# Optimization experiments

Hardware: AMD Instinct MI355X
Metric: run time of the kernel (lower is better)

Reference implementation:

```python
import jax, jax.numpy as jnp
import numpy as np
import functools

N_QUBITS = 4
N_LAYERS = 2
DIM = 2 ** N_QUBITS  # 16


def _cx_full(c, t, n):
    # Full 2^n x 2^n CX(control=c, target=t); Qiskit ordering: qubit 0 = LSB,
    # so kron list is ordered qubit n-1 (leftmost) ... qubit 0 (rightmost).
    P0 = np.diag([1.0, 0.0]); P1 = np.diag([0.0, 1.0])
    X = np.array([[0.0, 1.0], [1.0, 0.0]])
    ops0 = [np.eye(2)] * n; ops0[n - 1 - c] = P0
    ops1 = [np.eye(2)] * n; ops1[n - 1 - c] = P1; ops1[n - 1 - t] = X
    return functools.reduce(np.kron, ops0) + functools.reduce(np.kron, ops1)

# CX chain: CX(0,1), CX(1,2), CX(2,3) applied in circuit order (last applied is leftmost)
_chain = np.eye(DIM)
for _i in range(N_QUBITS - 1):
    _chain = _cx_full(_i, _i + 1, N_QUBITS) @ _chain
CX_CHAIN = jnp.asarray(_chain, dtype=jnp.complex64)
# Odd-pair CX: i in range(1, n_qubits-1, 2)
_odd = np.eye(DIM)
for _i in range(1, N_QUBITS - 1, 2):
    _odd = _cx_full(_i, _i + 1, N_QUBITS) @ _odd
CX_ODD = jnp.asarray(_odd, dtype=jnp.complex64)


def _ry(t):
    c = jnp.cos(t / 2); s = jnp.sin(t / 2)
    return jnp.stack([jnp.stack([c, -s]), jnp.stack([s, c])]).astype(jnp.complex64)


def _rz(t):
    tc = t.astype(jnp.complex64)
    return jnp.diag(jnp.stack([jnp.exp(-0.5j * tc), jnp.exp(0.5j * tc)]))


def _stage(gate_fn, thetas):
    # thetas[i] acts on qubit i; kron ordered qubit n-1 ... qubit 0 (LSB rightmost)
    mats = [gate_fn(thetas[q]) for q in range(N_QUBITS - 1, -1, -1)]
    return functools.reduce(jnp.kron, mats)


def _layer_unitary(theta):
    # theta: (3*N_QUBITS,); per qubit i: RY(theta[3i]) ... RZ(theta[3i+1]) ... RY(theta[3i+2])
    ry_a = _stage(_ry, theta[0::3])
    rz_b = _stage(_rz, theta[1::3])
    ry_c = _stage(_ry, theta[2::3])
    return ry_c @ CX_ODD @ rz_b @ CX_CHAIN @ ry_a


def _quantum_mp(qf, mp_params):
    # qf: (N, n_qubits) real encoded features -> per-node statevector simulation
    v = qf / (jnp.linalg.norm(qf, axis=1, keepdims=True) + 1e-8)
    state = jnp.pad(v, ((0, 0), (0, DIM - N_QUBITS)))  # (N, 16)
    state = state / (jnp.linalg.norm(state, axis=1, keepdims=True) + 1e-8)
    state = state / jnp.linalg.norm(state, axis=1, keepdims=True)
    state = state.astype(jnp.complex64)
    for layer in range(N_LAYERS):
        U = _layer_unitary(mp_params[layer * 3 * N_QUBITS:(layer + 1) * 3 * N_QUBITS])
        state = state @ U.T  # batched U @ |psi>
    return state[:, :N_QUBITS].real.astype(jnp.float32)


def setup_inputs() -> dict:
    key = jax.random.key(0)
    ks = jax.random.split(key, 11)
    N, D_IN, HID = 10000, 256, 128
    return {
        "node_features": jax.random.normal(ks[0], (N, D_IN), jnp.float32),
        "adjacency": jax.random.randint(ks[1], (N, N), 0, 2, jnp.int32),
        "W_e1": jax.random.normal(ks[2], (D_IN, HID), jnp.float32) * 0.05,
        "b_e1": jax.random.normal(ks[3], (HID,), jnp.float32) * 0.05,
        "W_e2": jax.random.normal(ks[4], (HID, N_QUBITS), jnp.float32) * 0.05,
        "b_e2": jax.random.normal(ks[5], (N_QUBITS,), jnp.float32) * 0.05,
        "mp_params": jax.random.normal(ks[6], (N_LAYERS * 3 * N_QUBITS,), jnp.float32) * 0.1,
        "W_d1": jax.random.normal(ks[7], (N_QUBITS, HID), jnp.float32) * 0.05,
        "b_d1": jax.random.normal(ks[8], (HID,), jnp.float32) * 0.05,
        "W_d2": jax.random.normal(ks[9], (HID, HID), jnp.float32) * 0.05,
        "b_d2": jax.random.normal(ks[10], (HID,), jnp.float32) * 0.05,
    }


def reference(node_features, adjacency, W_e1, b_e1, W_e2, b_e2, mp_params, W_d1, b_d1, W_d2, b_d2):
    # Encoder: Linear -> ReLU -> Linear  => (N, n_qubits)
    qf = jnp.maximum(node_features @ W_e1 + b_e1, 0.0) @ W_e2 + b_e2
    # torch detaches both the encoded features and mp_params before the quantum sim
    qf = jax.lax.stop_gradient(qf)
    theta = jax.lax.stop_gradient(mp_params)
    # NOTE: aggregate_neighbors ignores neighbor_states entirely, so adjacency
    # does not influence the output (faithful to the source module).
    updated = _quantum_mp(qf, theta)  # (N, n_qubits)
    h = jnp.maximum(updated @ W_d1 + b_d1, 0.0)
    return h @ W_d2 + b_d2
```

## Files before the change

kernel.cpp:

```cpp
#include <hip/hip_runtime.h>
#include <math.h>

#define D_IN 256
#define HID  128
#define NQ   4
#define NPB  8


__device__ inline void apply_ry(float* re, float* im, int q, float t) {
    float c = cosf(0.5f * t), s = sinf(0.5f * t);
    int m = 1 << q;
    for (int i = 0; i < 16; ++i) {
        if (i & m) continue;
        int i1 = i | m;
        float r0 = re[i], m0 = im[i], r1 = re[i1], m1 = im[i1];
        re[i]  = c * r0 - s * r1;  im[i]  = c * m0 - s * m1;
        re[i1] = s * r0 + c * r1;  im[i1] = s * m0 + c * m1;
    }
}

__device__ inline void apply_rz(float* re, float* im, int q, float t) {
    float c = cosf(0.5f * t), s = sinf(0.5f * t);
    int m = 1 << q;
    for (int i = 0; i < 16; ++i) {
        float r = re[i], mm = im[i];
        if (i & m) { re[i] = r * c - mm * s; im[i] = mm * c + r * s; }
        else       { re[i] = r * c + mm * s; im[i] = mm * c - r * s; }
    }
}

__device__ inline void apply_cx(float* re, float* im, int c, int t) {
    int mc = 1 << c, mt = 1 << t;
    for (int i = 0; i < 16; ++i) {
        if ((i & mc) && !(i & mt)) {
            int i1 = i | mt;
            float r = re[i]; re[i] = re[i1]; re[i1] = r;
            float mm = im[i]; im[i] = im[i1]; im[i1] = mm;
        }
    }
}

__global__ void prelude_kernel(const float* __restrict__ mp,
                               const float* __restrict__ Wd1,
                               float* __restrict__ Weff) {
    __shared__ float M4[4][4];
    if (threadIdx.x == 0) {
        for (int b = 0; b < 4; ++b) {
            float re[16], im[16];
            for (int i = 0; i < 16; ++i) { re[i] = 0.f; im[i] = 0.f; }
            re[b] = 1.f;
            for (int L = 0; L < 2; ++L) {
                const float* th = mp + 12 * L;
                for (int q = 0; q < 4; ++q) apply_ry(re, im, q, th[3 * q + 0]);
                apply_cx(re, im, 0, 1);
                apply_cx(re, im, 1, 2);
                apply_cx(re, im, 2, 3);
                for (int q = 0; q < 4; ++q) apply_rz(re, im, q, th[3 * q + 1]);
                apply_cx(re, im, 1, 2);
                for (int q = 0; q < 4; ++q) apply_ry(re, im, q, th[3 * q + 2]);
            }
            for (int jj = 0; jj < 4; ++jj) M4[jj][b] = re[jj];
        }
    }
    __syncthreads();
    int j = threadIdx.x;
    for (int k = 0; k < 4; ++k) {
        float a = 0.f;
        for (int q = 0; q < 4; ++q) a += M4[q][k] * Wd1[q * HID + j];
        Weff[k * HID + j] = a;
    }
}


__global__ __launch_bounds__(128) void fused_gnn_kernel(
    const float* __restrict__ X,
    const float* __restrict__ We1, const float* __restrict__ be1,
    const float* __restrict__ We2, const float* __restrict__ be2,
    const float* __restrict__ Weff, const float* __restrict__ bd1,
    const float* __restrict__ Wd2, const float* __restrict__ bd2,
    float* __restrict__ out, int N)
{
    __shared__ float Xs[NPB][D_IN + 4];
    __shared__ float hs[NPB][HID + 4];
    __shared__ float qs[NPB][4];
    __shared__ float s4s[NPB][4];

    const int j  = threadIdx.x;
    const int n0 = blockIdx.x * NPB;

    for (int idx = j; idx < NPB * (D_IN / 4); idx += 128) {
        int n  = idx / (D_IN / 4);
        int kk = (idx % (D_IN / 4)) * 4;
        float4 v = make_float4(0.f, 0.f, 0.f, 0.f);
        if (n0 + n < N) v = *(const float4*)(X + (size_t)(n0 + n) * D_IN + kk);
        *(float4*)&Xs[n][kk] = v;
    }
    __syncthreads();

    float acc[NPB];
    {
        float b1 = be1[j];
        #pragma unroll
        for (int n = 0; n < NPB; ++n) acc[n] = b1;
    }
    for (int k = 0; k < D_IN; k += 4) {
        float w0 = We1[(k + 0) * HID + j];
        float w1 = We1[(k + 1) * HID + j];
        float w2 = We1[(k + 2) * HID + j];
        float w3 = We1[(k + 3) * HID + j];
        #pragma unroll
        for (int n = 0; n < NPB; ++n) {
            float4 x = *(const float4*)&Xs[n][k];
            acc[n] = fmaf(x.x, w0, acc[n]);
            acc[n] = fmaf(x.y, w1, acc[n]);
            acc[n] = fmaf(x.z, w2, acc[n]);
            acc[n] = fmaf(x.w, w3, acc[n]);
        }
    }
    #pragma unroll
    for (int n = 0; n < NPB; ++n) hs[n][j] = fmaxf(acc[n], 0.f);
    __syncthreads();

    if (j < NPB * 4) {
        int n = j >> 2, c = j & 3;
        float a = be2[c];
        #pragma unroll 8
        for (int k = 0; k < HID; ++k) a = fmaf(hs[n][k], We2[k * 4 + c], a);
        qs[n][c] = a;
    }
    __syncthreads();

    if (j < NPB) {
        float q0 = qs[j][0], q1 = qs[j][1], q2 = qs[j][2], q3 = qs[j][3];
        float nn  = sqrtf(q0 * q0 + q1 * q1 + q2 * q2 + q3 * q3);
        float inv = 1.f / (nn + 1e-8f);
        q0 *= inv; q1 *= inv; q2 *= inv; q3 *= inv;
        nn  = sqrtf(q0 * q0 + q1 * q1 + q2 * q2 + q3 * q3);
        inv = 1.f / (nn + 1e-8f);
        q0 *= inv; q1 *= inv; q2 *= inv; q3 *= inv;
        nn  = sqrtf(q0 * q0 + q1 * q1 + q2 * q2 + q3 * q3);
        inv = 1.f / nn;
        s4s[j][0] = q0 * inv; s4s[j][1] = q1 * inv;
        s4s[j][2] = q2 * inv; s4s[j][3] = q3 * inv;
    }
    __syncthreads();

    float hv[NPB];
    {
        float w0 = Weff[0 * HID + j], w1 = Weff[1 * HID + j];
        float w2 = Weff[2 * HID + j], w3 = Weff[3 * HID + j];
        float bd = bd1[j];
        #pragma unroll
        for (int n = 0; n < NPB; ++n) {
            float a = bd;
            a = fmaf(s4s[n][0], w0, a);
            a = fmaf(s4s[n][1], w1, a);
            a = fmaf(s4s[n][2], w2, a);
            a = fmaf(s4s[n][3], w3, a);
            hv[n] = fmaxf(a, 0.f);
        }
    }
    __syncthreads();
    #pragma unroll
    for (int n = 0; n < NPB; ++n) hs[n][j] = hv[n];
    __syncthreads();

    float o[NPB];
    {
        float b2 = bd2[j];
        #pragma unroll
        for (int n = 0; n < NPB; ++n) o[n] = b2;
    }
    for (int k = 0; k < HID; k += 4) {
        float w0 = Wd2[(k + 0) * HID + j];
        float w1 = Wd2[(k + 1) * HID + j];
        float w2 = Wd2[(k + 2) * HID + j];
        float w3 = Wd2[(k + 3) * HID + j];
        #pragma unroll
        for (int n = 0; n < NPB; ++n) {
            float4 h4 = *(const float4*)&hs[n][k];
            o[n] = fmaf(h4.x, w0, o[n]);
            o[n] = fmaf(h4.y, w1, o[n]);
            o[n] = fmaf(h4.z, w2, o[n]);
            o[n] = fmaf(h4.w, w3, o[n]);
        }
    }
    #pragma unroll
    for (int n = 0; n < NPB; ++n) {
        if (n0 + n < N) out[(size_t)(n0 + n) * HID + j] = o[n];
    }
}


extern "C" void kernel_launch(void* const* d_in, const int* in_sizes, int n_in,
                              void* d_out, int out_size, void* d_ws, size_t ws_size,
                              hipStream_t stream) {
    const float* X   = (const float*)d_in[0];
    const float* We1 = (const float*)d_in[2];
    const float* be1 = (const float*)d_in[3];
    const float* We2 = (const float*)d_in[4];
    const float* be2 = (const float*)d_in[5];
    const float* mp  = (const float*)d_in[6];
    const float* Wd1 = (const float*)d_in[7];
    const float* bd1 = (const float*)d_in[8];
    const float* Wd2 = (const float*)d_in[9];
    const float* bd2 = (const float*)d_in[10];
    float* out  = (float*)d_out;
    float* Weff = (float*)d_ws;

    const int N = in_sizes[0] / D_IN;

    prelude_kernel<<<1, 128, 0, stream>>>(mp, Wd1, Weff);

    const int nblocks = (N + NPB - 1) / NPB;
    fused_gnn_kernel<<<nblocks, 128, 0, stream>>>(
        X, We1, be1, We2, be2, Weff, bd1, Wd2, bd2, out, N);
}
```

Before: 513.7 us.

## Fold quantum prelude into main kernel, recomputing 4x4 unitary per block

Removes the separate single-thread prelude launch. Each block now has four threads simulate the fixed circuit and build the 4x4 real submatrix, overlapped with the X tile load done by the other 64 threads. The small matrix is then applied to the normalized state before the Wd1 projection. Gate routines are templated and unrolled so the state stays in registers. The cost is redundant trig and circuit work in every block, and the X load now uses half the threads.

```diff
diff --git a/kernel.cpp b/kernel.cpp
--- a/kernel.cpp
+++ b/kernel.cpp
@@ -7,67 +7,39 @@
 #define NPB  8
 
 
-__device__ inline void apply_ry(float* re, float* im, int q, float t) {
+template<int Q>
+__device__ __forceinline__ void ry16(float re[16], float im[16], float t) {
     float c = cosf(0.5f * t), s = sinf(0.5f * t);
-    int m = 1 << q;
+    #pragma unroll
     for (int i = 0; i < 16; ++i) {
-        if (i & m) continue;
-        int i1 = i | m;
+        if (i & (1 << Q)) continue;
+        const int i1 = i | (1 << Q);
         float r0 = re[i], m0 = im[i], r1 = re[i1], m1 = im[i1];
         re[i]  = c * r0 - s * r1;  im[i]  = c * m0 - s * m1;
         re[i1] = s * r0 + c * r1;  im[i1] = s * m0 + c * m1;
     }
 }
 
-__device__ inline void apply_rz(float* re, float* im, int q, float t) {
+template<int Q>
+__device__ __forceinline__ void rz16(float re[16], float im[16], float t) {
     float c = cosf(0.5f * t), s = sinf(0.5f * t);
-    int m = 1 << q;
+    #pragma unroll
     for (int i = 0; i < 16; ++i) {
         float r = re[i], mm = im[i];
-        if (i & m) { re[i] = r * c - mm * s; im[i] = mm * c + r * s; }
-        else       { re[i] = r * c + mm * s; im[i] = mm * c - r * s; }
-    }
-}
-
-__device__ inline void apply_cx(float* re, float* im, int c, int t) {
-    int mc = 1 << c, mt = 1 << t;
+        if (i & (1 << Q)) { re[i] = r * c - mm * s; im[i] = mm * c + r * s; }
+        else              { re[i] = r * c + mm * s; im[i] = mm * c - r * s; }
+    }
+}
+
+template<int C, int T>
+__device__ __forceinline__ void cx16(float re[16], float im[16]) {
+    #pragma unroll
     for (int i = 0; i < 16; ++i) {
-        if ((i & mc) && !(i & mt)) {
-            int i1 = i | mt;
-            float r = re[i]; re[i] = re[i1]; re[i1] = r;
+        if ((i & (1 << C)) && !(i & (1 << T))) {
+            const int i1 = i | (1 << T);
+            float r  = re[i]; re[i] = re[i1]; re[i1] = r;
             float mm = im[i]; im[i] = im[i1]; im[i1] = mm;
         }
-    }
-}
-
-__global__ void prelude_kernel(const float* __restrict__ mp,
-                               const float* __restrict__ Wd1,
-                               float* __restrict__ Weff) {
-    __shared__ float M4[4][4];
-    if (threadIdx.x == 0) {
-        for (int b = 0; b < 4; ++b) {
-            float re[16], im[16];
-            for (int i = 0; i < 16; ++i) { re[i] = 0.f; im[i] = 0.f; }
-            re[b] = 1.f;
-            for (int L = 0; L < 2; ++L) {
-                const float* th = mp + 12 * L;
-                for (int q = 0; q < 4; ++q) apply_ry(re, im, q, th[3 * q + 0]);
-                apply_cx(re, im, 0, 1);
-                apply_cx(re, im, 1, 2);
-                apply_cx(re, im, 2, 3);
-                for (int q = 0; q < 4; ++q) apply_rz(re, im, q, th[3 * q + 1]);
-                apply_cx(re, im, 1, 2);
-                for (int q = 0; q < 4; ++q) apply_ry(re, im, q, th[3 * q + 2]);
-            }
-            for (int jj = 0; jj < 4; ++jj) M4[jj][b] = re[jj];
-        }
-    }
-    __syncthreads();
-    int j = threadIdx.x;
-    for (int k = 0; k < 4; ++k) {
-        float a = 0.f;
-        for (int q = 0; q < 4; ++q) a += M4[q][k] * Wd1[q * HID + j];
-        Weff[k * HID + j] = a;
     }
 }
 
@@ -76,24 +48,48 @@
     const float* __restrict__ X,
     const float* __restrict__ We1, const float* __restrict__ be1,
     const float* __restrict__ We2, const float* __restrict__ be2,
-    const float* __restrict__ Weff, const float* __restrict__ bd1,
+    const float* __restrict__ mp,  const float* __restrict__ Wd1,
+    const float* __restrict__ bd1,
     const float* __restrict__ Wd2, const float* __restrict__ bd2,
     float* __restrict__ out, int N)
 {
     __shared__ float Xs[NPB][D_IN + 4];
     __shared__ float hs[NPB][HID + 4];
     __shared__ float qs[NPB][4];
-    __shared__ float s4s[NPB][4];
+    __shared__ float t4s[NPB][4];
+    __shared__ float M4s[4][4];
 
     const int j  = threadIdx.x;
     const int n0 = blockIdx.x * NPB;
 
-    for (int idx = j; idx < NPB * (D_IN / 4); idx += 128) {
-        int n  = idx / (D_IN / 4);
-        int kk = (idx % (D_IN / 4)) * 4;
-        float4 v = make_float4(0.f, 0.f, 0.f, 0.f);
-        if (n0 + n < N) v = *(const float4*)(X + (size_t)(n0 + n) * D_IN + kk);
-        *(float4*)&Xs[n][kk] = v;
+    if (j < 64) {
+        for (int idx = j; idx < NPB * (D_IN / 4); idx += 64) {
+            int n  = idx / (D_IN / 4);
+            int kk = (idx % (D_IN / 4)) * 4;
+            float4 v = make_float4(0.f, 0.f, 0.f, 0.f);
+            if (n0 + n < N) v = *(const float4*)(X + (size_t)(n0 + n) * D_IN + kk);
+            *(float4*)&Xs[n][kk] = v;
+        }
+    }
+    if (j >= 64 && j < 68) {
+        const int b = j - 64;
+        float re[16], im[16];
+        #pragma unroll
+        for (int i = 0; i < 16; ++i) { re[i] = 0.f; im[i] = 0.f; }
+        re[b] = 1.f;
+        for (int L = 0; L < 2; ++L) {
+            const float* th = mp + 12 * L;
+            ry16<0>(re, im, th[0]);  ry16<1>(re, im, th[3]);
+            ry16<2>(re, im, th[6]);  ry16<3>(re, im, th[9]);
+            cx16<0, 1>(re, im); cx16<1, 2>(re, im); cx16<2, 3>(re, im);
+            rz16<0>(re, im, th[1]);  rz16<1>(re, im, th[4]);
+            rz16<2>(re, im, th[7]);  rz16<3>(re, im, th[10]);
+            cx16<1, 2>(re, im);
+            ry16<0>(re, im, th[2]);  ry16<1>(re, im, th[5]);
+            ry16<2>(re, im, th[8]);  ry16<3>(re, im, th[11]);
+        }
+        M4s[0][b] = re[0]; M4s[1][b] = re[1];
+        M4s[2][b] = re[2]; M4s[3][b] = re[3];
     }
     __syncthreads();
 
@@ -140,23 +136,27 @@
         q0 *= inv; q1 *= inv; q2 *= inv; q3 *= inv;
         nn  = sqrtf(q0 * q0 + q1 * q1 + q2 * q2 + q3 * q3);
         inv = 1.f / nn;
-        s4s[j][0] = q0 * inv; s4s[j][1] = q1 * inv;
-        s4s[j][2] = q2 * inv; s4s[j][3] = q3 * inv;
+        q0 *= inv; q1 *= inv; q2 *= inv; q3 *= inv;
+        #pragma unroll
+        for (int r = 0; r < 4; ++r) {
+            t4s[j][r] = M4s[r][0] * q0 + M4s[r][1] * q1
+                      + M4s[r][2] * q2 + M4s[r][3] * q3;
+        }
     }
     __syncthreads();
 
     float hv[NPB];
     {
-        float w0 = Weff[0 * HID + j], w1 = Weff[1 * HID + j];
-        float w2 = Weff[2 * HID + j], w3 = Weff[3 * HID + j];
+        float w0 = Wd1[0 * HID + j], w1 = Wd1[1 * HID + j];
+        float w2 = Wd1[2 * HID + j], w3 = Wd1[3 * HID + j];
         float bd = bd1[j];
         #pragma unroll
         for (int n = 0; n < NPB; ++n) {
             float a = bd;
-            a = fmaf(s4s[n][0], w0, a);
-            a = fmaf(s4s[n][1], w1, a);
-            a = fmaf(s4s[n][2], w2, a);
-            a = fmaf(s4s[n][3], w3, a);
+            a = fmaf(t4s[n][0], w0, a);
+            a = fmaf(t4s[n][1], w1, a);
+            a = fmaf(t4s[n][2], w2, a);
+            a = fmaf(t4s[n][3], w3, a);
             hv[n] = fmaxf(a, 0.f);
         }
     }
@@ -205,14 +205,11 @@
     const float* bd1 = (const float*)d_in[8];
     const float* Wd2 = (const float*)d_in[9];
     const float* bd2 = (const float*)d_in[10];
-    float* out  = (float*)d_out;
-    float* Weff = (float*)d_ws;
+    float* out = (float*)d_out;
+    (void)d_ws; (void)ws_size;
 
     const int N = in_sizes[0] / D_IN;
-
-    prelude_kernel<<<1, 128, 0, stream>>>(mp, Wd1, Weff);
-
     const int nblocks = (N + NPB - 1) / NPB;
     fused_gnn_kernel<<<nblocks, 128, 0, stream>>>(
-        X, We1, be1, We2, be2, Weff, bd1, Wd2, bd2, out, N);
-}
+        X, We1, be1, We2, be2, mp, Wd1, bd1, Wd2, bd2, out, N);
+}
```

Result: faster. 488.7 us (-4.9%).
